# Performance work log

Hardware: AMD Instinct MI355X
Metric: run time of the kernel (lower is better)

Reference implementation:

```python
import jax, jax.numpy as jnp
import numpy as np

TEMP = 0.05
DIAG_PENALTY = 1e12
EPS = 1e-8  # matches torch F.cosine_similarity eps


def setup_inputs() -> dict:
    key = jax.random.key(0)
    x = jax.random.normal(key, (8192, 768), dtype=jnp.float32)
    return {"x": x}


def reference(x):
    n = x.shape[0]
    # labels: swap adjacent pairs -> i - (i%2)*2 + 1  (i.e. i XOR 1)
    idx = jnp.arange(n)
    labels = idx - (idx % 2) * 2 + 1
    # cosine similarity matrix via normalize + GEMM (same math as broadcasted
    # F.cosine_similarity: dot(x_i, x_j) / (max(||x_i||,eps) * max(||x_j||,eps)))
    norms = jnp.maximum(jnp.linalg.norm(x, axis=-1, keepdims=True), EPS)
    xn = x / norms
    sim = xn @ xn.T                                   # [N, N]
    sim = sim - jnp.eye(n, dtype=sim.dtype) * DIAG_PENALTY
    logits = sim / TEMP
    # mean cross-entropy with stable log-softmax
    logp = jax.nn.log_softmax(logits, axis=-1)
    loss = -jnp.mean(jnp.take_along_axis(logp, labels[:, None], axis=-1))
    return loss
```

## Files before the change

### kernel.cpp

```cpp
#include <hip/hip_runtime.h>
#include <hip/hip_bf16.h>

#define N 8192
#define D 768
#define TEMP_INV 20.0f
#define NTILES 528

typedef __attribute__((ext_vector_type(4))) float f32x4;
typedef __attribute__((ext_vector_type(4))) int i32x4;
typedef __attribute__((ext_vector_type(8))) int i32x8;

#define SCALE1 0x7F7F7F7F


__global__ __launch_bounds__(256) void norm_kernel(
    const float* __restrict__ x, unsigned char* __restrict__ xn,
    float* __restrict__ rowsum) {
  int t = threadIdx.x, w = t >> 6, lane = t & 63;
  int row = blockIdx.x * 4 + w;
  const float4* xr = (const float4*)(x + (size_t)row * D);
  float4 v[3];
  v[0] = xr[lane];
  v[1] = xr[lane + 64];
  v[2] = xr[lane + 128];
  float ss = 0.0f;
#pragma unroll
  for (int i = 0; i < 3; ++i)
    ss += v[i].x * v[i].x + v[i].y * v[i].y + v[i].z * v[i].z + v[i].w * v[i].w;
#pragma unroll
  for (int m = 32; m; m >>= 1) ss += __shfl_xor(ss, m);
  float inv = 1.0f / fmaxf(sqrtf(ss), 1e-8f);
  unsigned int* xo = (unsigned int*)(xn + (size_t)row * D);
#pragma unroll
  for (int i = 0; i < 3; ++i) {
    int p = __builtin_amdgcn_cvt_pk_fp8_f32(v[i].x * inv, v[i].y * inv, 0, false);
    p = __builtin_amdgcn_cvt_pk_fp8_f32(v[i].z * inv, v[i].w * inv, p, true);
    xo[lane + 64 * i] = p;
  }
  if (t < 4) rowsum[blockIdx.x * 4 + t] = 0.0f;
}

__global__ __launch_bounds__(512, 2) void sim_kernel(
    const unsigned char* __restrict__ xn, float* __restrict__ rowsum,
    float* __restrict__ pos) {
  static const short stbase[37] = {
      0, 10, 26, 42, 58, 74, 90, 106, 122,
      132, 148, 164, 180, 196, 212, 228,
      238, 254, 270, 286, 302, 318,
      328, 344, 360, 376, 392,
      402, 418, 434, 450,
      460, 476, 492,
      502, 518,
      528};
  static const char sti[36] = {0,0,0,0,0,0,0,0, 1,1,1,1,1,1,1, 2,2,2,2,2,2,
                               3,3,3,3,3, 4,4,4,4, 5,5,5, 6,6, 7};
  static const char stj[36] = {0,1,2,3,4,5,6,7, 1,2,3,4,5,6,7, 2,3,4,5,6,7,
                               3,4,5,6,7, 4,5,6,7, 5,6,7, 6,7, 7};
  int b = blockIdx.x;
  int p = 66 * (b & 7) + (b >> 3);
  int s = 0;
  while ((int)stbase[s + 1] <= p) ++s;
  int wofs = p - stbase[s];
  int SI = sti[s], SJ = stj[s];
  int bi, bj;
  if (SI == SJ) {
    int di = 0, cum = 0;
    while (wofs >= cum + (4 - di)) { cum += 4 - di; ++di; }
    bi = SI * 4 + di;
    bj = SI * 4 + di + (wofs - cum);
  } else {
    bi = SI * 4 + (wofs >> 2);
    bj = SJ * 4 + (wofs & 3);
  }

  __shared__ i32x4 As4[2][2048];
  __shared__ i32x4 Bs4[2][2048];

  int t = threadIdx.x;
  int w = t >> 6, lane = t & 63;
  int q = lane >> 4, cl = lane & 15;
  int wm = w >> 2, wn = w & 3;

  f32x4 acc[8][4] = {};

  int ulog = (((t & 7) ^ ((t >> 3) & 7))) * 16;
  const unsigned char* Ab = xn + (size_t)(bi * 256 + (t >> 3)) * D + ulog;
  const unsigned char* Bb = xn + (size_t)(bj * 256 + (t >> 3)) * D + ulog;

  int u0 = (2 * q) ^ (cl & 7);
  int u1 = u0 ^ 1;

  auto stageA = [&](int buf, int k0) {
#pragma unroll
    for (int rr = 0; rr < 4; ++rr)
      __builtin_amdgcn_global_load_lds(
          (const __attribute__((address_space(1))) unsigned int*)(Ab + (size_t)(rr * 64) * D + k0),
          (__attribute__((address_space(3))) unsigned int*)(&As4[buf][rr * 512 + t]), 16, 0, 0);
  };
  auto stageB = [&](int buf, int k0) {
#pragma unroll
    for (int rr = 0; rr < 4; ++rr)
      __builtin_amdgcn_global_load_lds(
          (const __attribute__((address_space(1))) unsigned int*)(Bb + (size_t)(rr * 64) * D + k0),
          (__attribute__((address_space(3))) unsigned int*)(&Bs4[buf][rr * 512 + t]), 16, 0, 0);
  };

  stageA(0, 0);
  stageB(0, 0);
  asm volatile("s_waitcnt vmcnt(0)" ::: "memory");
  __builtin_amdgcn_s_barrier();
  __builtin_amdgcn_sched_barrier(0);

  union Frag { i32x8 v8; struct { i32x4 lo, hi; } pr; };

#pragma unroll
  for (int kc = 0; kc < 6; ++kc) {
    const int cur = kc & 1;
    const int k1 = (kc + 1) * 128;
    Frag a[4], a2[4], bb[2];

#pragma unroll
    for (int n = 0; n < 2; ++n) {
      int rowb = (wn * 64 + n * 16 + cl) * 8;
      bb[n].pr.lo = Bs4[cur][rowb + u0];
      bb[n].pr.hi = Bs4[cur][rowb + u1];
    }
#pragma unroll
    for (int m = 0; m < 4; ++m) {
      int rowb = (wm * 128 + m * 16 + cl) * 8;
      a[m].pr.lo = As4[cur][rowb + u0];
      a[m].pr.hi = As4[cur][rowb + u1];
    }
    if (kc < 5) stageA(cur ^ 1, k1);
    __builtin_amdgcn_s_barrier();
    asm volatile("s_waitcnt lgkmcnt(0)" ::: "memory");
    __builtin_amdgcn_sched_barrier(0);
    __builtin_amdgcn_s_setprio(1);
#pragma unroll
    for (int m = 0; m < 4; ++m)
#pragma unroll
      for (int n = 0; n < 2; ++n)
        acc[m][n] = __builtin_amdgcn_mfma_scale_f32_16x16x128_f8f6f4(
            a[m].v8, bb[n].v8, acc[m][n], 0, 0, 0, SCALE1, 0, SCALE1);
    __builtin_amdgcn_s_setprio(0);
    __builtin_amdgcn_s_barrier();
    __builtin_amdgcn_sched_barrier(0);

#pragma unroll
    for (int m = 0; m < 4; ++m) {
      int rowb = (wm * 128 + (m + 4) * 16 + cl) * 8;
      a2[m].pr.lo = As4[cur][rowb + u0];
      a2[m].pr.hi = As4[cur][rowb + u1];
    }
    if (kc < 5) stageB(cur ^ 1, k1);
    __builtin_amdgcn_s_barrier();
    asm volatile("s_waitcnt lgkmcnt(0)" ::: "memory");
    __builtin_amdgcn_sched_barrier(0);
    __builtin_amdgcn_s_setprio(1);
#pragma unroll
    for (int m = 0; m < 4; ++m)
#pragma unroll
      for (int n = 0; n < 2; ++n)
        acc[m + 4][n] = __builtin_amdgcn_mfma_scale_f32_16x16x128_f8f6f4(
            a2[m].v8, bb[n].v8, acc[m + 4][n], 0, 0, 0, SCALE1, 0, SCALE1);
    __builtin_amdgcn_s_setprio(0);
    __builtin_amdgcn_s_barrier();
    __builtin_amdgcn_sched_barrier(0);

#pragma unroll
    for (int n = 0; n < 2; ++n) {
      int rowb = (wn * 64 + (n + 2) * 16 + cl) * 8;
      bb[n].pr.lo = Bs4[cur][rowb + u0];
      bb[n].pr.hi = Bs4[cur][rowb + u1];
    }
    __builtin_amdgcn_s_barrier();
    asm volatile("s_waitcnt lgkmcnt(0)" ::: "memory");
    __builtin_amdgcn_sched_barrier(0);
    __builtin_amdgcn_s_setprio(1);
#pragma unroll
    for (int m = 0; m < 4; ++m)
#pragma unroll
      for (int n = 0; n < 2; ++n)
        acc[m][n + 2] = __builtin_amdgcn_mfma_scale_f32_16x16x128_f8f6f4(
            a[m].v8, bb[n].v8, acc[m][n + 2], 0, 0, 0, SCALE1, 0, SCALE1);
#pragma unroll
    for (int m = 0; m < 4; ++m)
#pragma unroll
      for (int n = 0; n < 2; ++n)
        acc[m + 4][n + 2] = __builtin_amdgcn_mfma_scale_f32_16x16x128_f8f6f4(
            a2[m].v8, bb[n].v8, acc[m + 4][n + 2], 0, 0, 0, SCALE1, 0, SCALE1);
    __builtin_amdgcn_s_setprio(0);
    if (kc < 5) {
      asm volatile("s_waitcnt vmcnt(0)" ::: "memory");
      __builtin_amdgcn_s_barrier();
      __builtin_amdgcn_sched_barrier(0);
    }
  }

  int gi0 = bi * 256 + wm * 128;
  int gj0 = bj * 256 + wn * 64;

  float rowp[8][4] = {};
  float colp[4] = {};

  if (bi == bj) {
#pragma unroll
    for (int m = 0; m < 8; ++m)
#pragma unroll
      for (int n = 0; n < 4; ++n)
#pragma unroll
        for (int r = 0; r < 4; ++r) {
          float sv = acc[m][n][r];
          int row = gi0 + m * 16 + q * 4 + r;
          int col = gj0 + n * 16 + cl;
          float e = __expf(TEMP_INV * sv - 20.0f);
          if (col == row) e = 0.0f;
          if (col == (row ^ 1)) pos[row] = TEMP_INV * sv;
          rowp[m][r] += e;
        }
  } else {
#pragma unroll
    for (int m = 0; m < 8; ++m)
#pragma unroll
      for (int n = 0; n < 4; ++n)
#pragma unroll
        for (int r = 0; r < 4; ++r) {
          float e = __expf(TEMP_INV * acc[m][n][r] - 20.0f);
          rowp[m][r] += e;
          colp[n] += e;
        }
  }

#pragma unroll
  for (int m = 0; m < 8; ++m)
#pragma unroll
    for (int r = 0; r < 4; ++r) {
      float v = rowp[m][r];
      v += __shfl_xor(v, 1);
      v += __shfl_xor(v, 2);
      v += __shfl_xor(v, 4);
      v += __shfl_xor(v, 8);
      if (cl == 0) atomicAdd(&rowsum[gi0 + m * 16 + q * 4 + r], v);
    }
  if (bi != bj) {
#pragma unroll
    for (int n = 0; n < 4; ++n) {
      float v = colp[n];
      v += __shfl_xor(v, 16);
      v += __shfl_xor(v, 32);
      if (q == 0) atomicAdd(&rowsum[gj0 + n * 16 + cl], v);
    }
  }
}

__global__ __launch_bounds__(1024) void loss_kernel(
    const float* __restrict__ rowsum, const float* __restrict__ pos,
    float* __restrict__ out) {
  int t = threadIdx.x;
  const float4* r4 = (const float4*)rowsum;
  const float4* p4 = (const float4*)pos;
  float acc = 0.0f;
#pragma unroll
  for (int it = 0; it < 2; ++it) {
    int i = t + it * 1024;
    float4 r = r4[i], pp = p4[i];
    acc += 80.0f + __logf(r.x) + __logf(r.y) + __logf(r.z) + __logf(r.w)
           - pp.x - pp.y - pp.z - pp.w;
  }
#pragma unroll
  for (int m = 32; m; m >>= 1) acc += __shfl_xor(acc, m);
  __shared__ float wsum[16];
  if ((t & 63) == 0) wsum[t >> 6] = acc;
  __syncthreads();
  if (t == 0) {
    float tot = 0.0f;
#pragma unroll
    for (int i = 0; i < 16; ++i) tot += wsum[i];
    out[0] = tot / (float)N;
  }
}

extern "C" void kernel_launch(void* const* d_in, const int* in_sizes, int n_in,
                              void* d_out, int out_size, void* d_ws, size_t ws_size,
                              hipStream_t stream) {
  const float* x = (const float*)d_in[0];
  float* rowsum = (float*)d_ws;
  float* pos = rowsum + N;
  unsigned char* xn = (unsigned char*)(rowsum + 2 * N + 16);

  norm_kernel<<<N / 4, 256, 0, stream>>>(x, xn, rowsum);
  sim_kernel<<<NTILES, 512, 0, stream>>>(xn, rowsum, pos);
  loss_kernel<<<1, 1024, 0, stream>>>(rowsum, pos, (float*)d_out);
}
```

Before: 151.7 us.

## Prefetch two K-chunks ahead with vmcnt-gated in-place refill of LDS buffers

Restructures the FP8 MFMA GEMM main loop so both LDS buffers are filled up front and each chunk is refilled two iterations ahead, writing into the buffer just consumed. A partial vmcnt(8) wait replaces the full drain at the end of every iteration. The sub-tile order changes so the B half and the A half of the current buffer are released early and reloaded while the remaining MFMAs run. This aims to hide global-to-LDS latency better, but it relies on precise vmcnt counting and barrier placement to avoid overwriting data still being read.

```diff
diff --git a/kernel.cpp b/kernel.cpp
--- a/kernel.cpp
+++ b/kernel.cpp
@@ -90,48 +90,51 @@
   int u0 = (2 * q) ^ (cl & 7);
   int u1 = u0 ^ 1;
 
-  auto stageA = [&](int buf, int k0) {
-#pragma unroll
-    for (int rr = 0; rr < 4; ++rr)
-      __builtin_amdgcn_global_load_lds(
-          (const __attribute__((address_space(1))) unsigned int*)(Ab + (size_t)(rr * 64) * D + k0),
-          (__attribute__((address_space(3))) unsigned int*)(&As4[buf][rr * 512 + t]), 16, 0, 0);
+  auto gA = [&](int buf, int r0, int k0) {
+    __builtin_amdgcn_global_load_lds(
+        (const __attribute__((address_space(1))) unsigned int*)(Ab + (size_t)r0 * D + k0),
+        (__attribute__((address_space(3))) unsigned int*)(&As4[buf][r0 * 8 + t]), 16, 0, 0);
+    __builtin_amdgcn_global_load_lds(
+        (const __attribute__((address_space(1))) unsigned int*)(Ab + (size_t)(r0 + 64) * D + k0),
+        (__attribute__((address_space(3))) unsigned int*)(&As4[buf][(r0 + 64) * 8 + t]), 16, 0, 0);
   };
-  auto stageB = [&](int buf, int k0) {
-#pragma unroll
-    for (int rr = 0; rr < 4; ++rr)
-      __builtin_amdgcn_global_load_lds(
-          (const __attribute__((address_space(1))) unsigned int*)(Bb + (size_t)(rr * 64) * D + k0),
-          (__attribute__((address_space(3))) unsigned int*)(&Bs4[buf][rr * 512 + t]), 16, 0, 0);
+  auto gB = [&](int buf, int r0, int k0) {
+    __builtin_amdgcn_global_load_lds(
+        (const __attribute__((address_space(1))) unsigned int*)(Bb + (size_t)r0 * D + k0),
+        (__attribute__((address_space(3))) unsigned int*)(&Bs4[buf][r0 * 8 + t]), 16, 0, 0);
+    __builtin_amdgcn_global_load_lds(
+        (const __attribute__((address_space(1))) unsigned int*)(Bb + (size_t)(r0 + 64) * D + k0),
+        (__attribute__((address_space(3))) unsigned int*)(&Bs4[buf][(r0 + 64) * 8 + t]), 16, 0, 0);
   };
 
-  stageA(0, 0);
-  stageB(0, 0);
-  asm volatile("s_waitcnt vmcnt(0)" ::: "memory");
-  __builtin_amdgcn_s_barrier();
-  __builtin_amdgcn_sched_barrier(0);
+  gB(0, 0, 0);   gB(0, 128, 0);   gA(0, 0, 0);   gA(0, 128, 0);
+  gB(1, 0, 128); gB(1, 128, 128); gA(1, 0, 128); gA(1, 128, 128);
 
   union Frag { i32x8 v8; struct { i32x4 lo, hi; } pr; };
 
 #pragma unroll
   for (int kc = 0; kc < 6; ++kc) {
     const int cur = kc & 1;
-    const int k1 = (kc + 1) * 128;
-    Frag a[4], a2[4], bb[2];
-
+    const int k2 = (kc + 2) * 128;
+    if (kc < 5) { asm volatile("s_waitcnt vmcnt(8)" ::: "memory"); }
+    else        { asm volatile("s_waitcnt vmcnt(0)" ::: "memory"); }
+    __builtin_amdgcn_s_barrier();
+    __builtin_amdgcn_sched_barrier(0);
+
+    Frag a_lo[4], a_hi[4], b_lo[2], b_hi[2];
+
+#pragma unroll
+    for (int m = 0; m < 4; ++m) {
+      int rowb = (wm * 128 + m * 16 + cl) * 8;
+      a_lo[m].pr.lo = As4[cur][rowb + u0];
+      a_lo[m].pr.hi = As4[cur][rowb + u1];
+    }
 #pragma unroll
     for (int n = 0; n < 2; ++n) {
       int rowb = (wn * 64 + n * 16 + cl) * 8;
-      bb[n].pr.lo = Bs4[cur][rowb + u0];
-      bb[n].pr.hi = Bs4[cur][rowb + u1];
-    }
-#pragma unroll
-    for (int m = 0; m < 4; ++m) {
-      int rowb = (wm * 128 + m * 16 + cl) * 8;
-      a[m].pr.lo = As4[cur][rowb + u0];
-      a[m].pr.hi = As4[cur][rowb + u1];
-    }
-    if (kc < 5) stageA(cur ^ 1, k1);
+      b_lo[n].pr.lo = Bs4[cur][rowb + u0];
+      b_lo[n].pr.hi = Bs4[cur][rowb + u1];
+    }
     __builtin_amdgcn_s_barrier();
     asm volatile("s_waitcnt lgkmcnt(0)" ::: "memory");
     __builtin_amdgcn_sched_barrier(0);
@@ -141,7 +144,27 @@
 #pragma unroll
       for (int n = 0; n < 2; ++n)
         acc[m][n] = __builtin_amdgcn_mfma_scale_f32_16x16x128_f8f6f4(
-            a[m].v8, bb[n].v8, acc[m][n], 0, 0, 0, SCALE1, 0, SCALE1);
+            a_lo[m].v8, b_lo[n].v8, acc[m][n], 0, 0, 0, SCALE1, 0, SCALE1);
+    __builtin_amdgcn_s_setprio(0);
+    __builtin_amdgcn_s_barrier();
+    __builtin_amdgcn_sched_barrier(0);
+
+#pragma unroll
+    for (int n = 0; n < 2; ++n) {
+      int rowb = (wn * 64 + (n + 2) * 16 + cl) * 8;
+      b_hi[n].pr.lo = Bs4[cur][rowb + u0];
+      b_hi[n].pr.hi = Bs4[cur][rowb + u1];
+    }
+    __builtin_amdgcn_s_barrier();
+    asm volatile("s_waitcnt lgkmcnt(0)" ::: "memory");
+    __builtin_amdgcn_sched_barrier(0);
+    __builtin_amdgcn_s_setprio(1);
+#pragma unroll
+    for (int m = 0; m < 4; ++m)
+#pragma unroll
+      for (int n = 0; n < 2; ++n)
+        acc[m][n + 2] = __builtin_amdgcn_mfma_scale_f32_16x16x128_f8f6f4(
+            a_lo[m].v8, b_hi[n].v8, acc[m][n + 2], 0, 0, 0, SCALE1, 0, SCALE1);
     __builtin_amdgcn_s_setprio(0);
     __builtin_amdgcn_s_barrier();
     __builtin_amdgcn_sched_barrier(0);
@@ -149,10 +172,10 @@
 #pragma unroll
     for (int m = 0; m < 4; ++m) {
       int rowb = (wm * 128 + (m + 4) * 16 + cl) * 8;
-      a2[m].pr.lo = As4[cur][rowb + u0];
-      a2[m].pr.hi = As4[cur][rowb + u1];
-    }
-    if (kc < 5) stageB(cur ^ 1, k1);
+      a_hi[m].pr.lo = As4[cur][rowb + u0];
+      a_hi[m].pr.hi = As4[cur][rowb + u1];
+    }
+    if (kc < 4) { gB(cur, 0, k2); gB(cur, 128, k2); }
     __builtin_amdgcn_s_barrier();
     asm volatile("s_waitcnt lgkmcnt(0)" ::: "memory");
     __builtin_amdgcn_sched_barrier(0);
@@ -162,39 +185,20 @@
 #pragma unroll
       for (int n = 0; n < 2; ++n)
         acc[m + 4][n] = __builtin_amdgcn_mfma_scale_f32_16x16x128_f8f6f4(
-            a2[m].v8, bb[n].v8, acc[m + 4][n], 0, 0, 0, SCALE1, 0, SCALE1);
-    __builtin_amdgcn_s_setprio(0);
-    __builtin_amdgcn_s_barrier();
-    __builtin_amdgcn_sched_barrier(0);
-
-#pragma unroll
-    for (int n = 0; n < 2; ++n) {
-      int rowb = (wn * 64 + (n + 2) * 16 + cl) * 8;
-      bb[n].pr.lo = Bs4[cur][rowb + u0];
-      bb[n].pr.hi = Bs4[cur][rowb + u1];
-    }
-    __builtin_amdgcn_s_barrier();
-    asm volatile("s_waitcnt lgkmcnt(0)" ::: "memory");
-    __builtin_amdgcn_sched_barrier(0);
-    __builtin_amdgcn_s_setprio(1);
-#pragma unroll
-    for (int m = 0; m < 4; ++m)
-#pragma unroll
-      for (int n = 0; n < 2; ++n)
-        acc[m][n + 2] = __builtin_amdgcn_mfma_scale_f32_16x16x128_f8f6f4(
-            a[m].v8, bb[n].v8, acc[m][n + 2], 0, 0, 0, SCALE1, 0, SCALE1);
+            a_hi[m].v8, b_lo[n].v8, acc[m + 4][n], 0, 0, 0, SCALE1, 0, SCALE1);
+    __builtin_amdgcn_s_setprio(0);
+    __builtin_amdgcn_s_barrier();
+    __builtin_amdgcn_sched_barrier(0);
+
+    if (kc < 4) { gA(cur, 0, k2); gA(cur, 128, k2); }
+    __builtin_amdgcn_s_setprio(1);
 #pragma unroll
     for (int m = 0; m < 4; ++m)
 #pragma unroll
       for (int n = 0; n < 2; ++n)
         acc[m + 4][n + 2] = __builtin_amdgcn_mfma_scale_f32_16x16x128_f8f6f4(
-            a2[m].v8, bb[n].v8, acc[m + 4][n + 2], 0, 0, 0, SCALE1, 0, SCALE1);
-    __builtin_amdgcn_s_setprio(0);
-    if (kc < 5) {
-      asm volatile("s_waitcnt vmcnt(0)" ::: "memory");
-      __builtin_amdgcn_s_barrier();
-      __builtin_amdgcn_sched_barrier(0);
-    }
+            a_hi[m].v8, b_hi[n].v8, acc[m + 4][n + 2], 0, 0, 0, SCALE1, 0, SCALE1);
+    __builtin_amdgcn_s_setprio(0);
   }
 
   int gi0 = bi * 256 + wm * 128;
```

Result: faster. 142.7 us (-5.9%).
